# Optimization experiments

Hardware: AMD Instinct MI355X
Metric: run time of the kernel (lower is better)

## Reference

```python
import jax, jax.numpy as jnp
import numpy as np

# Dims: B=16 graphs, T=354 timesteps (l_max), N=64 nodes, H=128 model dim, NS=32 complex SSM modes

def setup_inputs() -> dict:
    key = jax.random.key(0)
    ks = jax.random.split(key, 10)
    B, T, N, H, NS = 16, 354, 64, 128, 32
    x = jax.random.normal(ks[0], (B, T, N), jnp.float32)
    W_in = jax.random.normal(ks[1], (H, 1), jnp.float32) * 0.5
    b_in = jnp.zeros((H,), jnp.float32)
    # S4D params: timescales log-uniform in [1e-3, 1e-1], A = -1/2 + i*pi*n (S4D-Lin init)
    log_dt = (jnp.log(0.001) + jax.random.uniform(ks[2], (H,), jnp.float32) * (jnp.log(0.1) - jnp.log(0.001))).astype(jnp.float32)
    A_re = -0.5 * jnp.ones((H, NS), jnp.float32)
    A_im = jnp.broadcast_to(np.pi * jnp.arange(NS, dtype=jnp.float32), (H, NS)).astype(jnp.float32) + 0.0
    C_re = jax.random.normal(ks[3], (H, NS), jnp.float32) * (0.5 ** 0.5)
    C_im = jax.random.normal(ks[4], (H, NS), jnp.float32) * (0.5 ** 0.5)
    D = jax.random.normal(ks[5], (H,), jnp.float32)
    W_out = jax.random.normal(ks[6], (2 * H, H), jnp.float32) * (1.0 / np.sqrt(H))
    b_out = jnp.zeros((2 * H,), jnp.float32)
    W_cls = jax.random.normal(ks[7], (1, H), jnp.float32) * (1.0 / np.sqrt(H))
    b_cls = jnp.zeros((1,), jnp.float32)
    return {"x": x, "W_in": W_in, "b_in": b_in, "log_dt": log_dt, "A_re": A_re, "A_im": A_im,
            "C_re": C_re, "C_im": C_im, "D": D, "W_out": W_out, "b_out": b_out,
            "W_cls": W_cls, "b_cls": b_cls}


def reference(x, W_in, b_in, log_dt, A_re, A_im, C_re, C_im, D, W_out, b_out, W_cls, b_cls):
    B, T, N = x.shape
    H = W_in.shape[0]
    # (B,T,N) -> (B*N, T, 1) per-node scalar series
    u = x.transpose(0, 2, 1).reshape(B * N, T, 1)
    u = u * W_in[:, 0] + b_in            # input_proj: (BN, T, H)
    u = u.transpose(0, 2, 1)             # transposed layout: (BN, H, L)
    # ---- S4D kernel (ZOH discretization, conjugate-pair 2*Re trick) ----
    dt = jnp.exp(log_dt)                 # (H,)
    A = A_re + 1j * A_im                 # (H, NS) complex64
    dtA = A * dt[:, None]                # (H, NS)
    C = C_re + 1j * C_im
    C_disc = C * (jnp.exp(dtA) - 1.0) / A
    l = jnp.arange(T)
    vand = jnp.exp(dtA[:, :, None] * l)  # Vandermonde (H, NS, L)
    K = 2.0 * jnp.real(jnp.einsum('hn,hnl->hl', C_disc, vand))  # (H, L)
    # ---- FFT causal long convolution + skip ----
    n_fft = 2 * T
    yf = jnp.fft.rfft(u, n_fft) * jnp.fft.rfft(K, n_fft)
    y = jnp.fft.irfft(yf, n_fft)[..., :T] + D[:, None] * u   # (BN, H, L)
    y = jax.nn.gelu(y)
    # dropout: identity at inference
    # ---- position-wise output linear H -> 2H, then GLU over channels ----
    g = jnp.einsum('bhl,gh->bgl', y, W_out) + b_out[:, None]  # (BN, 2H, L)
    z = g[:, :H] * jax.nn.sigmoid(g[:, H:])                    # (BN, H, L)
    # ---- pooling + classifier ----
    node_feats = z.mean(axis=-1).reshape(B, N, H)
    graph_feats = node_feats.mean(axis=1)                      # (B, H)
    logits = graph_feats @ W_cls.T + b_cls                     # (B, 1)
    return logits
```

## Files before the change

kernel.cpp:

```cpp
#include <hip/hip_runtime.h>
#include <hip/hip_bf16.h>


#define B_  16
#define T_  354
#define N_  64
#define H_  128
#define NS_ 32
#define BN_ (B_*N_)
#define TP_ 384
#define KW_ 512
#define PAD_ 136
#define G_  8
#define NG_ ((T_ + G_ - 1) / G_)

typedef __attribute__((ext_vector_type(8))) short bf16x8;
typedef __attribute__((ext_vector_type(4))) float f32x4;

static __device__ __forceinline__ unsigned short f32_to_bf16(float f) {
    unsigned int u = __float_as_uint(f);
    unsigned int r = 0x7FFFu + ((u >> 16) & 1u);
    return (unsigned short)((u + r) >> 16);
}

static __device__ __forceinline__ void gload_lds4(const void* g, void* l) {
    __builtin_amdgcn_global_load_lds(
        (const __attribute__((address_space(1))) unsigned int*)g,
        (__attribute__((address_space(3))) unsigned int*)l, 4, 0, 0);
}

static __device__ __forceinline__ float gelu_f(float v) {
    float v2 = v * v;
    float x  = v * fmaf(0.0713548162726f, v2, 1.5957691216057f);
    float sg = 1.0f / (1.0f + __expf(-x));
    return v * sg;
}

__global__ __launch_bounds__(512) void k_pre(
        const float* __restrict__ log_dt,
        const float* __restrict__ A_re, const float* __restrict__ A_im,
        const float* __restrict__ C_re, const float* __restrict__ C_im,
        const float* __restrict__ b_in, const float* __restrict__ D,
        const float* __restrict__ x, const float* __restrict__ W_out,
        unsigned short* __restrict__ Krev, float* __restrict__ koff,
        unsigned short* __restrict__ xbf, unsigned short* __restrict__ Wbf) {
    if (blockIdx.x >= H_) {
        int id = (blockIdx.x - H_) * 512 + threadIdx.x;
        if (id < T_ * BN_) {
            int t  = id >> 10;
            int bn = id & 1023;
            float v = x[(bn >> 6) * (T_ * N_) + t * N_ + (bn & 63)];
            xbf[bn * TP_ + t] = f32_to_bf16(v);
        } else {
            int i = id - T_ * BN_;
            if (i < 2 * H_ * H_) Wbf[i] = f32_to_bf16(W_out[i]);
        }
        return;
    }

    const int h = blockIdx.x;
    const int l = threadIdx.x;

    float val = 0.0f;
    if (l < T_) {
        float dt = expf(log_dt[h]);
        float fl = (float)l;
#pragma unroll 4
        for (int m = 0; m < NS_; m++) {
            float are = A_re[h * NS_ + m], aim = A_im[h * NS_ + m];
            float dre = are * dt, dim = aim * dt;
            float er  = expf(dre);
            float c1, s1; __sincosf(dim, &s1, &c1);
            float e_re = er * c1, e_im = er * s1;
            float m_re = e_re - 1.0f, m_im = e_im;
            float inv  = 1.0f / (are * are + aim * aim);
            float q_re = (m_re * are + m_im * aim) * inv;
            float q_im = (m_im * are - m_re * aim) * inv;
            float c_r = C_re[h * NS_ + m], c_i = C_im[h * NS_ + m];
            float cdre = c_r * q_re - c_i * q_im;
            float cdim = c_r * q_im + c_i * q_re;
            float el = expf(dre * fl);
            float cl, sl; __sincosf(dim * fl, &sl, &cl);
            val += el * (cdre * cl - cdim * sl);
        }
        val *= 2.0f;
        if (l == 0) val += D[h];
    }

    __shared__ float sc[512];
    sc[l] = (l < T_) ? val : 0.0f;
    __syncthreads();
    for (int off = 1; off < 512; off <<= 1) {
        float add = (l >= off) ? sc[l - off] : 0.0f;
        __syncthreads();
        sc[l] += add;
        __syncthreads();
    }

    if (l < T_) {
        koff[l * H_ + h] = b_in[h] * sc[l];
        unsigned short bv = f32_to_bf16(val);
#pragma unroll
        for (int r = 0; r < 8; r++)
            Krev[((size_t)r * H_ + h) * KW_ + (T_ - 1 - l) + r] = bv;
    }
}

__global__ __launch_bounds__(256, 2) void k_fused(
        const unsigned short* __restrict__ xbf,
        const unsigned short* __restrict__ Krev,
        const float* __restrict__ koff,
        const float* __restrict__ W_in,
        const unsigned short* __restrict__ Wbf,
        const float* __restrict__ b_out,
        float* __restrict__ node_sum) {
    __shared__ unsigned short x_lds[64 * PAD_];
    __shared__ unsigned short k_lds[128 * PAD_];

    const int tid  = threadIdx.x;
    const int w    = tid >> 6;
    const int lane = tid & 63;
    const int q    = lane >> 4;
    const int l16  = lane & 15;
    const int bn0  = blockIdx.x * 64;
    const int tg0  = blockIdx.y * G_;

    float win[2][4], bo1[2][4], bo2[2][4];
#pragma unroll
    for (int mt = 0; mt < 2; mt++)
#pragma unroll
        for (int rr = 0; rr < 4; rr++) {
            int hj = 32 * w + 16 * mt + 4 * q + rr;
            win[mt][rr] = W_in[hj];
            bo1[mt][rr] = b_out[hj];
            bo2[mt][rr] = b_out[128 + hj];
        }

    f32x4 zacc[2][4];
#pragma unroll
    for (int mt = 0; mt < 2; mt++)
#pragma unroll
        for (int nt = 0; nt < 4; nt++) zacc[mt][nt] = (f32x4){0.f, 0.f, 0.f, 0.f};

    for (int g = 0; g < G_; g++) {
        const int t = tg0 + g;
        if (t >= T_) break;
        const int nkb = (t >> 7) + 1;

        float ko[2][4];
#pragma unroll
        for (int mt = 0; mt < 2; mt++)
#pragma unroll
            for (int rr = 0; rr < 4; rr++)
                ko[mt][rr] = koff[t * H_ + 32 * w + 16 * mt + 4 * q + rr];

        f32x4 cacc[2][4];
#pragma unroll
        for (int mt = 0; mt < 2; mt++)
#pragma unroll
            for (int nt = 0; nt < 4; nt++) cacc[mt][nt] = (f32x4){0.f, 0.f, 0.f, 0.f};

        for (int kb = 0; kb < nkb; kb++) {
            const int tau0 = kb << 7;
            const int L    = 353 - t + tau0;
            const int cp   = (-L) & 7;
            const int kshi = min(3, (t - tau0) >> 5);
            __syncthreads();
#pragma unroll
            for (int i = 0; i < 16; i++) {
                int r = w * 16 + i;
                gload_lds4(xbf + (size_t)(bn0 + r) * TP_ + tau0 + lane * 2,
                           &x_lds[r * PAD_]);
            }
#pragma unroll 8
            for (int i = 0; i < 32; i++) {
                int hr = w * 32 + i;
                gload_lds4(Krev + ((size_t)cp * H_ + hr) * KW_ + (L + cp) + lane * 2,
                           &k_lds[hr * PAD_]);
            }
            __syncthreads();

            for (int ks = 0; ks <= kshi; ks++) {
                bf16x8 af[2], bf[4];
#pragma unroll
                for (int mt = 0; mt < 2; mt++)
                    af[mt] = *(const bf16x8*)&k_lds[(32 * w + 16 * mt + l16) * PAD_ + ks * 32 + q * 8];
#pragma unroll
                for (int nt = 0; nt < 4; nt++)
                    bf[nt] = *(const bf16x8*)&x_lds[(16 * nt + l16) * PAD_ + ks * 32 + q * 8];
#pragma unroll
                for (int mt = 0; mt < 2; mt++)
#pragma unroll
                    for (int nt = 0; nt < 4; nt++)
                        cacc[mt][nt] = __builtin_amdgcn_mfma_f32_16x16x32_bf16(
                            af[mt], bf[nt], cacc[mt][nt], 0, 0, 0);
            }
        }

        bf16x8 wfrag[4][4];
#pragma unroll
        for (int mt = 0; mt < 4; mt++) {
            int jb = 32 * w + 16 * (mt & 1) + 128 * (mt >> 1);
#pragma unroll
            for (int ks = 0; ks < 4; ks++)
                wfrag[mt][ks] = *(const bf16x8*)(Wbf + (size_t)(jb + l16) * H_ + ks * 32 + q * 8);
        }

        __syncthreads();
#pragma unroll
        for (int mt = 0; mt < 2; mt++)
#pragma unroll
            for (int nt = 0; nt < 4; nt++) {
                unsigned short pk[4];
#pragma unroll
                for (int rr = 0; rr < 4; rr++) {
                    float v = fmaf(cacc[mt][nt][rr], win[mt][rr], ko[mt][rr]);
                    pk[rr] = f32_to_bf16(gelu_f(v));
                }
                *(uint2*)&x_lds[(16 * nt + l16) * PAD_ + 32 * w + 16 * mt + 4 * q]
                    = *(const uint2*)pk;
            }
        __syncthreads();

        f32x4 gacc[4][4];
#pragma unroll
        for (int mt = 0; mt < 4; mt++)
#pragma unroll
            for (int nt = 0; nt < 4; nt++) gacc[mt][nt] = (f32x4){0.f, 0.f, 0.f, 0.f};
#pragma unroll
        for (int ks = 0; ks < 4; ks++) {
            bf16x8 yf[4];
#pragma unroll
            for (int nt = 0; nt < 4; nt++)
                yf[nt] = *(const bf16x8*)&x_lds[(16 * nt + l16) * PAD_ + ks * 32 + q * 8];
#pragma unroll
            for (int mt = 0; mt < 4; mt++)
#pragma unroll
                for (int nt = 0; nt < 4; nt++)
                    gacc[mt][nt] = __builtin_amdgcn_mfma_f32_16x16x32_bf16(
                        wfrag[mt][ks], yf[nt], gacc[mt][nt], 0, 0, 0);
        }

#pragma unroll
        for (int mt = 0; mt < 2; mt++)
#pragma unroll
            for (int nt = 0; nt < 4; nt++)
#pragma unroll
                for (int rr = 0; rr < 4; rr++) {
                    float a  = gacc[mt][nt][rr] + bo1[mt][rr];
                    float bs = gacc[mt + 2][nt][rr] + bo2[mt][rr];
                    float sg = 1.0f / (1.0f + __expf(-bs));
                    zacc[mt][nt][rr] += a * sg;
                }
    }

#pragma unroll
    for (int mt = 0; mt < 2; mt++)
#pragma unroll
        for (int nt = 0; nt < 4; nt++)
#pragma unroll
            for (int rr = 0; rr < 4; rr++) {
                int bn = bn0 + 16 * nt + l16;
                int j  = 32 * w + 16 * mt + 4 * q + rr;
                atomicAdd(&node_sum[bn * H_ + j], zacc[mt][nt][rr]);
            }
}

__global__ void k_cls(const float* __restrict__ node_sum,
                      const float* __restrict__ W_cls, const float* __restrict__ b_cls,
                      float* __restrict__ out) {
    const int b = blockIdx.x, tid = threadIdx.x;
    float s = 0.0f;
    for (int i = tid; i < N_ * H_; i += 256)
        s += node_sum[b * (N_ * H_) + i] * W_cls[i & (H_ - 1)];
    __shared__ float red[256];
    red[tid] = s;
    __syncthreads();
    for (int off = 128; off > 0; off >>= 1) {
        if (tid < off) red[tid] += red[tid + off];
        __syncthreads();
    }
    if (tid == 0) out[b] = red[0] * (1.0f / (354.0f * 64.0f)) + b_cls[0];
}

extern "C" void kernel_launch(void* const* d_in, const int* in_sizes, int n_in,
                              void* d_out, int out_size, void* d_ws, size_t ws_size,
                              hipStream_t stream) {
    const float* x      = (const float*)d_in[0];
    const float* W_in   = (const float*)d_in[1];
    const float* b_in   = (const float*)d_in[2];
    const float* log_dt = (const float*)d_in[3];
    const float* A_re   = (const float*)d_in[4];
    const float* A_im   = (const float*)d_in[5];
    const float* C_re   = (const float*)d_in[6];
    const float* C_im   = (const float*)d_in[7];
    const float* D      = (const float*)d_in[8];
    const float* W_out  = (const float*)d_in[9];
    const float* b_out  = (const float*)d_in[10];
    const float* W_cls  = (const float*)d_in[11];
    const float* b_cls  = (const float*)d_in[12];

    char* ws = (char*)d_ws;
    float*          node_sum = (float*)(ws + 0);
    unsigned short* xbf      = (unsigned short*)(ws + 524288);
    unsigned short* Krev     = (unsigned short*)(ws + 1310720);
    float*          koff     = (float*)(ws + 2359296);
    unsigned short* Wbf      = (unsigned short*)(ws + 2540544);

    hipMemsetAsync(ws, 0, 2359296, stream);
    const int prep_blocks = (T_ * BN_ + 2 * H_ * H_ + 511) / 512;
    k_pre<<<dim3(H_ + prep_blocks), dim3(512), 0, stream>>>(
        log_dt, A_re, A_im, C_re, C_im, b_in, D, x, W_out, Krev, koff, xbf, Wbf);
    k_fused<<<dim3(BN_ / 64, NG_), dim3(256), 0, stream>>>(
        xbf, Krev, koff, W_in, Wbf, b_out, node_sum);
    k_cls<<<dim3(B_), dim3(256), 0, stream>>>(node_sum, W_cls, b_cls, (float*)d_out);
}
```

Before: 285.4 us.

## Split fused conv+GLU kernel into separate conv and GLU kernels via bf16 buffer

Unfuses the convolution and the output-linear/GLU stages. k_conv writes gelu'd activations to a global bf16 buffer Y, and a new k_glu kernel reads them back to do the H->2H matmul, GLU and pooling. The aim is to cut register pressure so more blocks fit per CU (launch bounds raised to 3 and 4) and to give each stage its own time-grouping (4 vs 16). The x-to-bf16 transpose in k_pre now goes through shared memory with vectorized loads and stores. In exchange the activations take an extra global-memory round trip, roughly 93 MB written and read back.

New measurement: 243.9 us. -14.6%, faster.

```diff
diff --git a/kernel.cpp b/kernel.cpp
--- a/kernel.cpp
+++ b/kernel.cpp
@@ -11,8 +11,11 @@
 #define TP_ 384
 #define KW_ 512
 #define PAD_ 136
-#define G_  8
-#define NG_ ((T_ + G_ - 1) / G_)
+#define GC_ 4
+#define NGC_ ((T_ + GC_ - 1) / GC_)
+#define GT_ 16
+#define NGT_ ((T_ + GT_ - 1) / GT_)
+#define WB_ ((2 * H_ * H_) / 512)
 
 typedef __attribute__((ext_vector_type(8))) short bf16x8;
 typedef __attribute__((ext_vector_type(4))) float f32x4;
@@ -44,23 +47,40 @@
         const float* __restrict__ x, const float* __restrict__ W_out,
         unsigned short* __restrict__ Krev, float* __restrict__ koff,
         unsigned short* __restrict__ xbf, unsigned short* __restrict__ Wbf) {
-    if (blockIdx.x >= H_) {
-        int id = (blockIdx.x - H_) * 512 + threadIdx.x;
-        if (id < T_ * BN_) {
-            int t  = id >> 10;
-            int bn = id & 1023;
-            float v = x[(bn >> 6) * (T_ * N_) + t * N_ + (bn & 63)];
-            xbf[bn * TP_ + t] = f32_to_bf16(v);
-        } else {
-            int i = id - T_ * BN_;
-            if (i < 2 * H_ * H_) Wbf[i] = f32_to_bf16(W_out[i]);
-        }
+    const int blk = blockIdx.x;
+    const int tid = threadIdx.x;
+
+    if (blk >= H_ + 96) {
+        int id = (blk - H_ - 96) * 512 + tid;
+        if (id < 2 * H_ * H_) Wbf[id] = f32_to_bf16(W_out[id]);
         return;
     }
-
-    const int h = blockIdx.x;
-    const int l = threadIdx.x;
-
+    if (blk >= H_) {
+        __shared__ float xt[64][68];
+        int idx = blk - H_;
+        int bt = idx / 6, tt = idx % 6;
+        int r  = tid >> 3, fc = tid & 7;
+        int t  = tt * 64 + r;
+        float4 v0 = make_float4(0.f, 0.f, 0.f, 0.f), v1 = v0;
+        if (t < T_) {
+            const float* xp = x + ((size_t)bt * T_ + t) * N_ + fc * 8;
+            v0 = *(const float4*)xp;
+            v1 = *(const float4*)(xp + 4);
+        }
+        *(float4*)&xt[r][fc * 8]     = v0;
+        *(float4*)&xt[r][fc * 8 + 4] = v1;
+        __syncthreads();
+        int n = tid >> 3, tc = tid & 7;
+        unsigned short pk[8];
+#pragma unroll
+        for (int k = 0; k < 8; k++) pk[k] = f32_to_bf16(xt[tc * 8 + k][n]);
+        *(uint4*)(xbf + (size_t)(bt * 64 + n) * TP_ + tt * 64 + tc * 8)
+            = *(const uint4*)pk;
+        return;
+    }
+
+    const int h = blk;
+    const int l = tid;
     float val = 0.0f;
     if (l < T_) {
         float dt = expf(log_dt[h]);
@@ -106,14 +126,12 @@
     }
 }
 
-__global__ __launch_bounds__(256, 2) void k_fused(
+__global__ __launch_bounds__(256, 3) void k_conv(
         const unsigned short* __restrict__ xbf,
         const unsigned short* __restrict__ Krev,
         const float* __restrict__ koff,
         const float* __restrict__ W_in,
-        const unsigned short* __restrict__ Wbf,
-        const float* __restrict__ b_out,
-        float* __restrict__ node_sum) {
+        unsigned short* __restrict__ Y) {
     __shared__ unsigned short x_lds[64 * PAD_];
     __shared__ unsigned short k_lds[128 * PAD_];
 
@@ -123,26 +141,16 @@
     const int q    = lane >> 4;
     const int l16  = lane & 15;
     const int bn0  = blockIdx.x * 64;
-    const int tg0  = blockIdx.y * G_;
-
-    float win[2][4], bo1[2][4], bo2[2][4];
+    const int tg0  = blockIdx.y * GC_;
+
+    float win[2][4];
 #pragma unroll
     for (int mt = 0; mt < 2; mt++)
 #pragma unroll
-        for (int rr = 0; rr < 4; rr++) {
-            int hj = 32 * w + 16 * mt + 4 * q + rr;
-            win[mt][rr] = W_in[hj];
-            bo1[mt][rr] = b_out[hj];
-            bo2[mt][rr] = b_out[128 + hj];
-        }
-
-    f32x4 zacc[2][4];
-#pragma unroll
-    for (int mt = 0; mt < 2; mt++)
-#pragma unroll
-        for (int nt = 0; nt < 4; nt++) zacc[mt][nt] = (f32x4){0.f, 0.f, 0.f, 0.f};
-
-    for (int g = 0; g < G_; g++) {
+        for (int rr = 0; rr < 4; rr++)
+            win[mt][rr] = W_in[32 * w + 16 * mt + 4 * q + rr];
+
+    for (int g = 0; g < GC_; g++) {
         const int t = tg0 + g;
         if (t >= T_) break;
         const int nkb = (t >> 7) + 1;
@@ -197,15 +205,6 @@
             }
         }
 
-        bf16x8 wfrag[4][4];
-#pragma unroll
-        for (int mt = 0; mt < 4; mt++) {
-            int jb = 32 * w + 16 * (mt & 1) + 128 * (mt >> 1);
-#pragma unroll
-            for (int ks = 0; ks < 4; ks++)
-                wfrag[mt][ks] = *(const bf16x8*)(Wbf + (size_t)(jb + l16) * H_ + ks * 32 + q * 8);
-        }
-
         __syncthreads();
 #pragma unroll
         for (int mt = 0; mt < 2; mt++)
@@ -222,19 +221,78 @@
             }
         __syncthreads();
 
-        f32x4 gacc[4][4];
-#pragma unroll
-        for (int mt = 0; mt < 4; mt++)
+#pragma unroll
+        for (int i = 0; i < 4; i++) {
+            int c    = i * 256 + tid;
+            int row  = c >> 4;
+            int col8 = (c & 15) * 8;
+            uint4 v = *(const uint4*)&x_lds[row * PAD_ + col8];
+            *(uint4*)(Y + ((size_t)t * BN_ + bn0 + row) * H_ + col8) = v;
+        }
+    }
+}
+
+__global__ __launch_bounds__(256, 4) void k_glu(
+        const unsigned short* __restrict__ Y,
+        const unsigned short* __restrict__ Wbf,
+        const float* __restrict__ b_out,
+        float* __restrict__ node_sum) {
+    __shared__ unsigned short Yt[64 * PAD_];
+
+    const int tid  = threadIdx.x;
+    const int w    = tid >> 6;
+    const int lane = tid & 63;
+    const int q    = lane >> 4;
+    const int l16  = lane & 15;
+    const int jg   = blockIdx.x & 1;
+    const int bn0  = (blockIdx.x >> 1) * 64;
+    const int tg0  = blockIdx.y * GT_;
+    const int jlow = jg * 64 + w * 16;
+    const int jhigh = jlow + 128;
+
+    bf16x8 wfrag[2][4];
+#pragma unroll
+    for (int ks = 0; ks < 4; ks++) {
+        wfrag[0][ks] = *(const bf16x8*)(Wbf + (size_t)(jlow  + l16) * H_ + ks * 32 + q * 8);
+        wfrag[1][ks] = *(const bf16x8*)(Wbf + (size_t)(jhigh + l16) * H_ + ks * 32 + q * 8);
+    }
+    float bo1[4], bo2[4];
+#pragma unroll
+    for (int rr = 0; rr < 4; rr++) {
+        bo1[rr] = b_out[jlow  + 4 * q + rr];
+        bo2[rr] = b_out[jhigh + 4 * q + rr];
+    }
+
+    f32x4 zacc[4];
+#pragma unroll
+    for (int nt = 0; nt < 4; nt++) zacc[nt] = (f32x4){0.f, 0.f, 0.f, 0.f};
+
+    for (int g = 0; g < GT_; g++) {
+        const int t = tg0 + g;
+        if (t >= T_) break;
+        __syncthreads();
+#pragma unroll
+        for (int i = 0; i < 16; i++) {
+            int r = w * 16 + i;
+            gload_lds4(Y + ((size_t)t * BN_ + bn0 + r) * H_ + lane * 2,
+                       &Yt[r * PAD_]);
+        }
+        __syncthreads();
+
+        f32x4 gacc[2][4];
+#pragma unroll
+        for (int mt = 0; mt < 2; mt++)
 #pragma unroll
             for (int nt = 0; nt < 4; nt++) gacc[mt][nt] = (f32x4){0.f, 0.f, 0.f, 0.f};
+
 #pragma unroll
         for (int ks = 0; ks < 4; ks++) {
             bf16x8 yf[4];
 #pragma unroll
             for (int nt = 0; nt < 4; nt++)
-                yf[nt] = *(const bf16x8*)&x_lds[(16 * nt + l16) * PAD_ + ks * 32 + q * 8];
-#pragma unroll
-            for (int mt = 0; mt < 4; mt++)
+                yf[nt] = *(const bf16x8*)&Yt[(16 * nt + l16) * PAD_ + ks * 32 + q * 8];
+#pragma unroll
+            for (int mt = 0; mt < 2; mt++)
 #pragma unroll
                 for (int nt = 0; nt < 4; nt++)
                     gacc[mt][nt] = __builtin_amdgcn_mfma_f32_16x16x32_bf16(
@@ -242,28 +300,24 @@
         }
 
 #pragma unroll
-        for (int mt = 0; mt < 2; mt++)
-#pragma unroll
-            for (int nt = 0; nt < 4; nt++)
-#pragma unroll
-                for (int rr = 0; rr < 4; rr++) {
-                    float a  = gacc[mt][nt][rr] + bo1[mt][rr];
-                    float bs = gacc[mt + 2][nt][rr] + bo2[mt][rr];
-                    float sg = 1.0f / (1.0f + __expf(-bs));
-                    zacc[mt][nt][rr] += a * sg;
-                }
-    }
-
-#pragma unroll
-    for (int mt = 0; mt < 2; mt++)
-#pragma unroll
         for (int nt = 0; nt < 4; nt++)
 #pragma unroll
             for (int rr = 0; rr < 4; rr++) {
-                int bn = bn0 + 16 * nt + l16;
-                int j  = 32 * w + 16 * mt + 4 * q + rr;
-                atomicAdd(&node_sum[bn * H_ + j], zacc[mt][nt][rr]);
-            }
+                float a  = gacc[0][nt][rr] + bo1[rr];
+                float bs = gacc[1][nt][rr] + bo2[rr];
+                float sg = 1.0f / (1.0f + __expf(-bs));
+                zacc[nt][rr] += a * sg;
+            }
+    }
+
+#pragma unroll
+    for (int nt = 0; nt < 4; nt++)
+#pragma unroll
+        for (int rr = 0; rr < 4; rr++) {
+            int bn = bn0 + 16 * nt + l16;
+            int j  = jlow + 4 * q + rr;
+            atomicAdd(&node_sum[bn * H_ + j], zacc[nt][rr]);
+        }
 }
 
 __global__ void k_cls(const float* __restrict__ node_sum,
@@ -302,16 +356,18 @@
 
     char* ws = (char*)d_ws;
     float*          node_sum = (float*)(ws + 0);
-    unsigned short* xbf      = (unsigned short*)(ws + 524288);
-    unsigned short* Krev     = (unsigned short*)(ws + 1310720);
-    float*          koff     = (float*)(ws + 2359296);
+    unsigned short* Krev     = (unsigned short*)(ws + 524288);
+    float*          koff     = (float*)(ws + 1572864);
+    unsigned short* xbf      = (unsigned short*)(ws + 1754112);
     unsigned short* Wbf      = (unsigned short*)(ws + 2540544);
-
-    hipMemsetAsync(ws, 0, 2359296, stream);
-    const int prep_blocks = (T_ * BN_ + 2 * H_ * H_ + 511) / 512;
-    k_pre<<<dim3(H_ + prep_blocks), dim3(512), 0, stream>>>(
+    unsigned short* Y        = (unsigned short*)(ws + 2606080);
+
+    hipMemsetAsync(ws, 0, 1572864, stream);
+    k_pre<<<dim3(H_ + 96 + WB_), dim3(512), 0, stream>>>(
         log_dt, A_re, A_im, C_re, C_im, b_in, D, x, W_out, Krev, koff, xbf, Wbf);
-    k_fused<<<dim3(BN_ / 64, NG_), dim3(256), 0, stream>>>(
-        xbf, Krev, koff, W_in, Wbf, b_out, node_sum);
+    k_conv<<<dim3(BN_ / 64, NGC_), dim3(256), 0, stream>>>(
+        xbf, Krev, koff, W_in, Y);
+    k_glu<<<dim3(2 * BN_ / 64, NGT_), dim3(256), 0, stream>>>(
+        Y, Wbf, b_out, node_sum);
     k_cls<<<dim3(B_), dim3(256), 0, stream>>>(node_sum, W_cls, b_cls, (float*)d_out);
 }
```
